# Kernel tuning notes

Measured on AMD Instinct MI355X. Metric: run time of the kernel, lower is better.

The kernel has to match this reference:

```python
import jax, jax.numpy as jnp
import numpy as np

MAX_LEN, BATCH, D_IN, D_H = 512, 128, 512, 512


def setup_inputs() -> dict:
    key = jax.random.key(0)
    ks = jax.random.split(key, 9)
    s_in = 1.0 / np.sqrt(D_IN)
    s_h = 1.0 / np.sqrt(D_H)
    return {
        "seq": jax.random.normal(ks[0], (MAX_LEN, BATCH, D_IN), jnp.float32),
        "W_iz": jax.random.normal(ks[1], (D_H, D_IN), jnp.float32) * s_in,
        "b_iz": jax.random.normal(ks[2], (D_H,), jnp.float32) * s_in,
        "W_in": jax.random.normal(ks[3], (D_H, D_IN), jnp.float32) * s_in,
        "b_in": jax.random.normal(ks[4], (D_H,), jnp.float32) * s_in,
        "W_hz": jax.random.normal(ks[5], (D_H, D_H), jnp.float32) * s_h,
        "b_hz": jax.random.normal(ks[6], (D_H,), jnp.float32) * s_h,
        "W_hn": jax.random.normal(ks[7], (D_H, D_H), jnp.float32) * s_h,
        "b_hn": jax.random.normal(ks[8], (D_H,), jnp.float32) * s_h,
    }


def reference(seq, W_iz, b_iz, W_in, b_in, W_hz, b_hz, W_hn, b_hn):
    # Precompute input projections for all timesteps in one big GEMM each.
    # iz, inn: [max_len, batch, hidden]
    iz = jnp.einsum("tbi,hi->tbh", seq, W_iz) + b_iz
    inn = jnp.einsum("tbi,hi->tbh", seq, W_in) + b_in
    h0 = jnp.zeros((seq.shape[1], W_hz.shape[0]), seq.dtype)

    def step(h_prev, xs):
        iz_t, in_t = xs
        z_t = jax.nn.sigmoid(iz_t + h_prev @ W_hz.T + b_hz)
        # NOTE: original module sets r_t = ones, so no reset gating.
        n_t = jnp.tanh(in_t + (h_prev @ W_hn.T + b_hn))
        h_t = (1.0 - z_t) * n_t + z_t * h_prev
        return h_t, h_t

    _, H = jax.lax.scan(step, h0, (iz, inn))  # H: [max_len, batch, hidden]
    return H[None]  # [1, max_len, batch, hidden] (H.unsqueeze(0))
```

## Files before the change

### kernel.cpp

```cpp
#include <hip/hip_runtime.h>
#include <stdint.h>

typedef _Float16 f16x8 __attribute__((ext_vector_type(8)));
typedef _Float16 f16x4 __attribute__((ext_vector_type(4)));
typedef float    f32x4 __attribute__((ext_vector_type(4)));
typedef unsigned int u32x4v __attribute__((ext_vector_type(4)));

#define T_LEN 512
#define RLX   __ATOMIC_RELAXED
#define AGT   __HIP_MEMORY_SCOPE_AGENT

union PK4 { _Float16 h[4]; unsigned long long q; };
union QZ  { unsigned long long q; f16x4 v; };

__device__ __forceinline__ void gload_lds16(const void* gsrc, void* ldsdst) {
    auto g = (const __attribute__((address_space(1))) void*)(reinterpret_cast<uintptr_t>(gsrc));
    auto s = (__attribute__((address_space(3))) void*)(reinterpret_cast<uintptr_t>(ldsdst));
    __builtin_amdgcn_global_load_lds(g, s, 16, 0, 0);
}

__global__ __launch_bounds__(256) void prep_misc(
    const float* __restrict__ W_iz, const float* __restrict__ W_in,
    const float* __restrict__ W_hz, const float* __restrict__ W_hn,
    const float* __restrict__ b_iz, const float* __restrict__ b_in,
    const float* __restrict__ b_hz, const float* __restrict__ b_hn,
    _Float16* __restrict__ Wci, _Float16* __restrict__ Whc,
    float* __restrict__ bc, unsigned int* __restrict__ hbuf32)
{
    const int tid = blockIdx.x * 256 + threadIdx.x;
    if (tid < 131072) {
        const bool is_h = tid >= 65536;
        const int u = tid & 65535;
        const int e = u * 8;
        const int row = e >> 9;
        const int k = e & 511;
        const float* s;
        if (!is_h) s = (row < 512) ? (W_iz + (size_t)row * 512 + k)
                                   : (W_in + (size_t)(row - 512) * 512 + k);
        else       s = (row < 512) ? (W_hz + (size_t)row * 512 + k)
                                   : (W_hn + (size_t)(row - 512) * 512 + k);
        f32x4 a = *(const f32x4*)s;
        f32x4 b = *(const f32x4*)(s + 4);
        f16x8 o;
        o[0] = (_Float16)a[0]; o[1] = (_Float16)a[1];
        o[2] = (_Float16)a[2]; o[3] = (_Float16)a[3];
        o[4] = (_Float16)b[0]; o[5] = (_Float16)b[1];
        o[6] = (_Float16)b[2]; o[7] = (_Float16)b[3];
        _Float16* d = is_h ? Whc : Wci;
        *(f16x8*)(d + e) = o;
    } else if (tid < 132096) {
        const int j2 = tid - 131072;
        bc[j2] = (j2 < 512) ? (b_iz[j2] + b_hz[j2]) : (b_in[j2 - 512] + b_hn[j2 - 512]);
    } else if (tid < 164864) {
        const int u = tid - 132096;
        u32x4v z = {0u, 0u, 0u, 0u};
        *(u32x4v*)(hbuf32 + (size_t)u * 4) = z;
    }
}

__global__ __launch_bounds__(256) void gemm_proj(
    const float* __restrict__ A,
    const _Float16* __restrict__ Bw,
    const float* __restrict__ bc,
    _Float16* Co)
{
    __shared__ _Float16 As[128 * 40];
    __shared__ _Float16 Bs[128 * 32];

    const int mt = blockIdx.x;
    const int nt = blockIdx.y;
    const int m0 = mt * 128, n0 = nt * 128;
    const int tid = threadIdx.x;
    const int w = tid >> 6, l = tid & 63;
    const int wr = w >> 1, wc = w & 1;
    const int lrow = l & 15, lk = l >> 4;

    f32x4 acc[4][4] = {};

    const int arow = tid >> 1;
    const int acol = (tid & 1) * 16;

    for (int kt = 0; kt < 16; ++kt) {
        const int k0 = kt * 32;
        if (kt) __syncthreads();
        const float* as = A + (size_t)(m0 + arow) * 512 + k0 + acol;
        f32x4 a0 = *(const f32x4*)as;
        f32x4 a1 = *(const f32x4*)(as + 4);
        f32x4 a2 = *(const f32x4*)(as + 8);
        f32x4 a3 = *(const f32x4*)(as + 12);
        f16x8 h0, h1;
#pragma unroll
        for (int e = 0; e < 4; ++e) {
            h0[e] = (_Float16)a0[e]; h0[4 + e] = (_Float16)a1[e];
            h1[e] = (_Float16)a2[e]; h1[4 + e] = (_Float16)a3[e];
        }
        *(f16x8*)&As[arow * 40 + acol] = h0;
        *(f16x8*)&As[arow * 40 + acol + 8] = h1;
#pragma unroll
        for (int i = 0; i < 2; ++i) {
            const int chunk = w * 2 + i;
            const _Float16* gsrc =
                Bw + (size_t)(n0 + chunk * 16 + (l >> 2)) * 512 + k0 + (l & 3) * 8;
            gload_lds16(gsrc, &Bs[chunk * 512]);
        }
        __syncthreads();
        f16x8 af[4], bf[4];
#pragma unroll
        for (int i = 0; i < 4; ++i) {
            af[i] = *(const f16x8*)&As[(wr * 64 + i * 16 + lrow) * 40 + lk * 8];
            bf[i] = *(const f16x8*)&Bs[(wc * 64 + i * 16 + lrow) * 32 + lk * 8];
        }
#pragma unroll
        for (int mi = 0; mi < 4; ++mi)
#pragma unroll
            for (int ni = 0; ni < 4; ++ni)
                acc[mi][ni] = __builtin_amdgcn_mfma_f32_16x16x32_f16(
                    bf[ni], af[mi], acc[mi][ni], 0, 0, 0);
    }
    const int gate = nt >> 2;
#pragma unroll
    for (int mi = 0; mi < 4; ++mi) {
#pragma unroll
        for (int p = 0; p < 2; ++p) {
            const int j2q0 = n0 + wc * 64 + p * 32 + 4 * lk;
            const f32x4 b0 = *(const f32x4*)&bc[j2q0];
            const f32x4 b1 = *(const f32x4*)&bc[j2q0 + 16];
            f16x8 o;
#pragma unroll
            for (int r = 0; r < 4; ++r) {
                o[r]     = (_Float16)(acc[mi][2 * p][r]     + b0[r]);
                o[4 + r] = (_Float16)(acc[mi][2 * p + 1][r] + b1[r]);
            }
            const int blk_s = (wr * 4 + mi) * 16 + (nt & 3) * 4 + wc * 2 + p;
            _Float16* dst = Co + ((((size_t)mt * 128 + blk_s) * 2 + gate) * 512) + l * 8;
            *(f16x8*)dst = o;
        }
    }
}

__global__ __launch_bounds__(512, 1) void gru_scan(
    const _Float16* __restrict__ Whc,
    const char* izb,
    float* Hout,
    unsigned int* hbuf32)
{
    __shared__ _Float16 hlds[2 * 16 * 512];

    const int blk  = blockIdx.x;
    const int g    = blk & 7;
    const int slot = blk >> 3;
    const int tid  = threadIdx.x;
    const int wv   = tid >> 6;
    const int l    = tid & 63;
    const int lrow = l & 15, lk = l >> 4;
    const int jbase = slot * 128 + wv * 16;
    const int jq    = jbase + 4 * lk;
    const int bg    = 16 * g + lrow;
    const int blk_s = 16 * g + 4 * slot + (wv >> 1);
    const int stage_b = tid >> 5;
    const int stage_jq = 4 * (tid & 31);

    f16x8 wz[16], wn[16];
#pragma unroll
    for (int s = 0; s < 16; ++s) {
        wz[s] = *(const f16x8*)&Whc[(size_t)(jbase + lrow) * 512 + s * 32 + lk * 8];
        wn[s] = *(const f16x8*)&Whc[(size_t)(512 + jbase + lrow) * 512 + s * 32 + lk * 8];
    }

    *(unsigned long long*)&hlds[(lrow * 512 + jq) ^ ((lrow & 7) << 3)] = 0ull;

    QZ ez, en, oz, on;
    {
        const char* r0 = izb + ((size_t)0 * 128 + blk_s) * 2048 + l * 16 + (wv & 1) * 8;
        ez.q = *(const unsigned long long*)r0;
        en.q = *(const unsigned long long*)(r0 + 1024);
        const char* r1 = izb + ((size_t)1 * 128 + blk_s) * 2048 + l * 16 + (wv & 1) * 8;
        oz.q = *(const unsigned long long*)r1;
        on.q = *(const unsigned long long*)(r1 + 1024);
    }

    float hm[4] = {0.f, 0.f, 0.f, 0.f};

    const unsigned long long* hb64base = (const unsigned long long*)hbuf32;

    auto step = [&](int t, QZ& cz, QZ& cn) {
        const int par = (t + 1) & 1;
        const int lp  = t & 1;
        const unsigned long long tp =
            (unsigned long long)(unsigned)t | ((unsigned long long)(unsigned)t << 32);

        const unsigned long long* hb64 = hb64base + (size_t)par * 32768;
        unsigned long long q0[3], q1[3];
        int pix[3];
#pragma unroll
        for (int i = 0; i < 3; ++i) {
            const int s_i = (slot + 1 + i) & 3;
            const int u32i = (16 * g + stage_b) * 512 + s_i * 128 + stage_jq;
            pix[i] = u32i >> 1;
            q0[i] = __hip_atomic_load(hb64 + pix[i],     RLX, AGT);
            q1[i] = __hip_atomic_load(hb64 + pix[i] + 1, RLX, AGT);
        }
        while (true) {
            unsigned long long x = 0;
#pragma unroll
            for (int i = 0; i < 3; ++i)
                x |= (q0[i] ^ tp) | (q1[i] ^ tp);
            if (__all((x & 0x0000FFFF0000FFFFull) == 0)) break;
#pragma unroll
            for (int i = 0; i < 3; ++i) {
                q0[i] = __hip_atomic_load(hb64 + pix[i],     RLX, AGT);
                q1[i] = __hip_atomic_load(hb64 + pix[i] + 1, RLX, AGT);
            }
        }

#pragma unroll
        for (int i = 0; i < 3; ++i) {
            const int s_i = (slot + 1 + i) & 3;
            const unsigned int w0 = ((unsigned int)(q0[i] >> 16)) & 0xFFFFu;
            const unsigned int w1 = (unsigned int)(q0[i] >> 48);
            const unsigned int w2 = ((unsigned int)(q1[i] >> 16)) & 0xFFFFu;
            const unsigned int w3 = (unsigned int)(q1[i] >> 48);
            const unsigned long long out =
                (unsigned long long)(w0 | (w1 << 16)) |
                ((unsigned long long)(w2 | (w3 << 16)) << 32);
            const int idx = (lp * 8192 + stage_b * 512 + s_i * 128 + stage_jq)
                            ^ ((stage_b & 7) << 3);
            *(unsigned long long*)&hlds[idx] = out;
        }

        __syncthreads();

        f32x4 az = {0.f, 0.f, 0.f, 0.f}, an = {0.f, 0.f, 0.f, 0.f};
        const int hbase = lp * 8192 + lrow * 512;
        const int sw = (lrow & 7) << 3;
#pragma unroll
        for (int s = 0; s < 16; ++s) {
            asm volatile("" : "+v"(wz[s]), "+v"(wn[s]));
            const f16x8 hf = *(const f16x8*)&hlds[(hbase + s * 32 + lk * 8) ^ sw];
            az = __builtin_amdgcn_mfma_f32_16x16x32_f16(wz[s], hf, az, 0, 0, 0);
            an = __builtin_amdgcn_mfma_f32_16x16x32_f16(wn[s], hf, an, 0, 0, 0);
        }

        PK4 own;
        f32x4 Hv;
#pragma unroll
        for (int r = 0; r < 4; ++r) {
            float zpre = az[r] + (float)cz.v[r];
            float npre = an[r] + (float)cn.v[r];
            zpre = fminf(fmaxf(zpre, -30.f), 30.f);
            const float z = 1.f / (1.f + __expf(-zpre));
            npre = fminf(fmaxf(npre, -15.f), 15.f);
            const float e2 = __expf(2.f * npre);
            const float n = (e2 - 1.f) / (e2 + 1.f);
            hm[r] = (1.f - z) * n + z * hm[r];
            Hv[r] = hm[r];
            own.h[r] = (_Float16)hm[r];
        }

        if (t + 2 < T_LEN) {
            const char* rec = izb + ((size_t)(t + 2) * 128 + blk_s) * 2048
                              + l * 16 + (wv & 1) * 8;
            cz.q = *(const unsigned long long*)rec;
            cn.q = *(const unsigned long long*)(rec + 1024);
        }
        __builtin_amdgcn_sched_barrier(0);

        *(unsigned long long*)
            &hlds[(((t + 1) & 1) * 8192 + lrow * 512 + jq) ^ ((lrow & 7) << 3)] = own.q;

        if (t < T_LEN - 1) {
            if (t + 2 < T_LEN) {
                asm volatile("s_waitcnt vmcnt(2)" ::: "memory");
            } else {
                asm volatile("s_waitcnt vmcnt(0)" ::: "memory");
            }
            __builtin_amdgcn_sched_barrier(0);
            const unsigned long long tagp =
                (unsigned long long)(unsigned)(t + 1) |
                ((unsigned long long)(unsigned)(t + 1) << 32);
            const unsigned long long d0 =
                ((own.q & 0xFFFFull) << 16) |
                (((own.q >> 16) & 0xFFFFull) << 48) | tagp;
            const unsigned long long d1 =
                (((own.q >> 32) & 0xFFFFull) << 16) |
                (((own.q >> 48) & 0xFFFFull) << 48) | tagp;
            unsigned long long* hw = (unsigned long long*)
                (hbuf32 + (size_t)(t & 1) * 65536 + (size_t)bg * 512 + jq);
            __hip_atomic_store(hw,     d0, RLX, AGT);
            __hip_atomic_store(hw + 1, d1, RLX, AGT);
        }

        *(f32x4*)&Hout[(size_t)t * 65536 + (size_t)bg * 512 + jq] = Hv;
    };

    for (int t = 0; t < T_LEN; t += 2) {
        step(t,     ez, en);
        step(t + 1, oz, on);
    }
}

extern "C" void kernel_launch(void* const* d_in, const int* in_sizes, int n_in,
                              void* d_out, int out_size, void* d_ws, size_t ws_size,
                              hipStream_t stream) {
    (void)in_sizes; (void)n_in; (void)out_size; (void)ws_size;
    const float* seq  = (const float*)d_in[0];
    const float* W_iz = (const float*)d_in[1];
    const float* b_iz = (const float*)d_in[2];
    const float* W_in = (const float*)d_in[3];
    const float* b_in = (const float*)d_in[4];
    const float* W_hz = (const float*)d_in[5];
    const float* b_hz = (const float*)d_in[6];
    const float* W_hn = (const float*)d_in[7];
    const float* b_hn = (const float*)d_in[8];

    char* ws = (char*)d_ws;
    _Float16*     Wci    = (_Float16*)(ws);
    _Float16*     Whc    = (_Float16*)(ws + 1048576);
    float*        bc     = (float*)   (ws + 2097152);
    unsigned int* hbuf32 = (unsigned int*)(ws + 2101248);

    prep_misc<<<644, 256, 0, stream>>>(W_iz, W_in, W_hz, W_hn,
                                       b_iz, b_in, b_hz, b_hn,
                                       Wci, Whc, bc, hbuf32);
    gemm_proj<<<dim3(512, 8), 256, 0, stream>>>(seq, Wci, bc, (_Float16*)d_out);
    gru_scan<<<32, 512, 0, stream>>>(Whc, (const char*)d_out, (float*)d_out, hbuf32);
}
```

Before: 1.827 ms.

## Spread GRU scan over 128 small blocks with recurrent weights staged in LDS

The recurrent scan moves from 32 blocks of 512 threads to 128 blocks of 128 threads. Each block now owns 32 hidden units for a 16-row batch group, and its W_hz/W_hn slice is loaded into LDS with global_load_lds instead of being held in registers. The aim is to use more compute units and cut per-block MFMA work per timestep. In exchange, each block must poll 15 peer slices instead of 3 in the cross-block h exchange, which raises spin-wait traffic and synchronisation latency on every step, and weights are reread from LDS on each step.

```diff
diff --git a/kernel.cpp b/kernel.cpp
--- a/kernel.cpp
+++ b/kernel.cpp
@@ -138,12 +138,13 @@
     }
 }
 
-__global__ __launch_bounds__(512, 1) void gru_scan(
+__global__ __launch_bounds__(128, 1) void gru_scan(
     const _Float16* __restrict__ Whc,
     const char* izb,
     float* Hout,
     unsigned int* hbuf32)
 {
+    __shared__ _Float16 wlds[64 * 512];
     __shared__ _Float16 hlds[2 * 16 * 512];
 
     const int blk  = blockIdx.x;
@@ -153,34 +154,36 @@
     const int wv   = tid >> 6;
     const int l    = tid & 63;
     const int lrow = l & 15, lk = l >> 4;
-    const int jbase = slot * 128 + wv * 16;
-    const int jq    = jbase + 4 * lk;
-    const int bg    = 16 * g + lrow;
-    const int blk_s = 16 * g + 4 * slot + (wv >> 1);
-    const int stage_b = tid >> 5;
-    const int stage_jq = 4 * (tid & 31);
-
-    f16x8 wz[16], wn[16];
-#pragma unroll
-    for (int s = 0; s < 16; ++s) {
-        wz[s] = *(const f16x8*)&Whc[(size_t)(jbase + lrow) * 512 + s * 32 + lk * 8];
-        wn[s] = *(const f16x8*)&Whc[(size_t)(512 + jbase + lrow) * 512 + s * 32 + lk * 8];
-    }
+    const int j0   = slot * 32;
+    const int jq   = j0 + wv * 16 + 4 * lk;
+    const int bg   = 16 * g + lrow;
+    const int blk_s = 16 * g + slot;
+    const int stage_b = tid >> 3;
+    const int stage_j = (tid & 7) * 4;
+
+    for (int gate = 0; gate < 2; ++gate)
+#pragma unroll
+        for (int s = 0; s < 16; ++s) {
+            const _Float16* gsrc = Whc +
+                (size_t)(gate * 512 + j0 + wv * 16 + lrow) * 512 + s * 32 + lk * 8;
+            gload_lds16(gsrc, &wlds[((wv * 2 + gate) * 16 + s) * 512]);
+        }
 
     *(unsigned long long*)&hlds[(lrow * 512 + jq) ^ ((lrow & 7) << 3)] = 0ull;
 
     QZ ez, en, oz, on;
     {
-        const char* r0 = izb + ((size_t)0 * 128 + blk_s) * 2048 + l * 16 + (wv & 1) * 8;
-        ez.q = *(const unsigned long long*)r0;
-        en.q = *(const unsigned long long*)(r0 + 1024);
-        const char* r1 = izb + ((size_t)1 * 128 + blk_s) * 2048 + l * 16 + (wv & 1) * 8;
-        oz.q = *(const unsigned long long*)r1;
-        on.q = *(const unsigned long long*)(r1 + 1024);
-    }
+        const char* rec = izb + (size_t)blk_s * 2048 + l * 16 + wv * 8;
+        ez.q = *(const unsigned long long*)(rec);
+        en.q = *(const unsigned long long*)(rec + 1024);
+        oz.q = *(const unsigned long long*)(rec + 262144);
+        on.q = *(const unsigned long long*)(rec + 262144 + 1024);
+    }
+
+    asm volatile("s_waitcnt vmcnt(0)" ::: "memory");
+    __syncthreads();
 
     float hm[4] = {0.f, 0.f, 0.f, 0.f};
-
     const unsigned long long* hb64base = (const unsigned long long*)hbuf32;
 
     auto step = [&](int t, QZ& cz, QZ& cn) {
@@ -190,12 +193,12 @@
             (unsigned long long)(unsigned)t | ((unsigned long long)(unsigned)t << 32);
 
         const unsigned long long* hb64 = hb64base + (size_t)par * 32768;
-        unsigned long long q0[3], q1[3];
-        int pix[3];
-#pragma unroll
-        for (int i = 0; i < 3; ++i) {
-            const int s_i = (slot + 1 + i) & 3;
-            const int u32i = (16 * g + stage_b) * 512 + s_i * 128 + stage_jq;
+        unsigned long long q0[15], q1[15];
+        int pix[15];
+#pragma unroll
+        for (int i = 0; i < 15; ++i) {
+            const int s_i = (slot + 1 + i) & 15;
+            const int u32i = (16 * g + stage_b) * 512 + s_i * 32 + stage_j;
             pix[i] = u32i >> 1;
             q0[i] = __hip_atomic_load(hb64 + pix[i],     RLX, AGT);
             q1[i] = __hip_atomic_load(hb64 + pix[i] + 1, RLX, AGT);
@@ -203,19 +206,19 @@
         while (true) {
             unsigned long long x = 0;
 #pragma unroll
-            for (int i = 0; i < 3; ++i)
+            for (int i = 0; i < 15; ++i)
                 x |= (q0[i] ^ tp) | (q1[i] ^ tp);
             if (__all((x & 0x0000FFFF0000FFFFull) == 0)) break;
 #pragma unroll
-            for (int i = 0; i < 3; ++i) {
+            for (int i = 0; i < 15; ++i) {
                 q0[i] = __hip_atomic_load(hb64 + pix[i],     RLX, AGT);
                 q1[i] = __hip_atomic_load(hb64 + pix[i] + 1, RLX, AGT);
             }
         }
 
 #pragma unroll
-        for (int i = 0; i < 3; ++i) {
-            const int s_i = (slot + 1 + i) & 3;
+        for (int i = 0; i < 15; ++i) {
+            const int s_i = (slot + 1 + i) & 15;
             const unsigned int w0 = ((unsigned int)(q0[i] >> 16)) & 0xFFFFu;
             const unsigned int w1 = (unsigned int)(q0[i] >> 48);
             const unsigned int w2 = ((unsigned int)(q1[i] >> 16)) & 0xFFFFu;
@@ -223,7 +226,7 @@
             const unsigned long long out =
                 (unsigned long long)(w0 | (w1 << 16)) |
                 ((unsigned long long)(w2 | (w3 << 16)) << 32);
-            const int idx = (lp * 8192 + stage_b * 512 + s_i * 128 + stage_jq)
+            const int idx = (lp * 8192 + stage_b * 512 + s_i * 32 + stage_j)
                             ^ ((stage_b & 7) << 3);
             *(unsigned long long*)&hlds[idx] = out;
         }
@@ -235,10 +238,11 @@
         const int sw = (lrow & 7) << 3;
 #pragma unroll
         for (int s = 0; s < 16; ++s) {
-            asm volatile("" : "+v"(wz[s]), "+v"(wn[s]));
-            const f16x8 hf = *(const f16x8*)&hlds[(hbase + s * 32 + lk * 8) ^ sw];
-            az = __builtin_amdgcn_mfma_f32_16x16x32_f16(wz[s], hf, az, 0, 0, 0);
-            an = __builtin_amdgcn_mfma_f32_16x16x32_f16(wn[s], hf, an, 0, 0, 0);
+            const f16x8 wzv = *(const f16x8*)&wlds[((wv * 2 + 0) * 16 + s) * 512 + l * 8];
+            const f16x8 wnv = *(const f16x8*)&wlds[((wv * 2 + 1) * 16 + s) * 512 + l * 8];
+            const f16x8 hf  = *(const f16x8*)&hlds[(hbase + s * 32 + lk * 8) ^ sw];
+            az = __builtin_amdgcn_mfma_f32_16x16x32_f16(wzv, hf, az, 0, 0, 0);
+            an = __builtin_amdgcn_mfma_f32_16x16x32_f16(wnv, hf, an, 0, 0, 0);
         }
 
         PK4 own;
@@ -259,7 +263,7 @@
 
         if (t + 2 < T_LEN) {
             const char* rec = izb + ((size_t)(t + 2) * 128 + blk_s) * 2048
-                              + l * 16 + (wv & 1) * 8;
+                              + l * 16 + wv * 8;
             cz.q = *(const unsigned long long*)rec;
             cn.q = *(const unsigned long long*)(rec + 1024);
         }
@@ -323,5 +327,5 @@
                                        b_iz, b_in, b_hz, b_hn,
                                        Wci, Whc, bc, hbuf32);
     gemm_proj<<<dim3(512, 8), 256, 0, stream>>>(seq, Wci, bc, (_Float16*)d_out);
-    gru_scan<<<32, 512, 0, stream>>>(Whc, (const char*)d_out, (float*)d_out, hbuf32);
-}
+    gru_scan<<<128, 128, 0, stream>>>(Whc, (const char*)d_out, (float*)d_out, hbuf32);
+}
```

Result: slower. 2.483 ms (+36.0%).

## Split GRU scan across 64 blocks of 256 threads with weights staged in LDS

Applied to the files above, without the earlier changes.

The recurrent scan now runs on 64 workgroups of 4 waves instead of 32 of 8, so each block owns 64 hidden columns and exchanges h with 7 peer slots instead of 3. Recurrent weights move from registers into 128 KB of LDS, loaded asynchronously via global_load_lds, and the h buffer drops double-buffering in favour of an extra barrier before each refill. This spreads the per-step matmul over more CUs to shorten the serial critical path. In exchange there are more cross-block flag polls per step, extra LDS weight reads on every step, and an added barrier.

```diff
diff --git a/kernel.cpp b/kernel.cpp
--- a/kernel.cpp
+++ b/kernel.cpp
@@ -138,13 +138,14 @@
     }
 }
 
-__global__ __launch_bounds__(512, 1) void gru_scan(
+__global__ __launch_bounds__(256, 1) void gru_scan(
     const _Float16* __restrict__ Whc,
     const char* izb,
     float* Hout,
     unsigned int* hbuf32)
 {
-    __shared__ _Float16 hlds[2 * 16 * 512];
+    __shared__ _Float16 wlds[65536];
+    __shared__ _Float16 hlds[8192];
 
     const int blk  = blockIdx.x;
     const int g    = blk & 7;
@@ -153,49 +154,52 @@
     const int wv   = tid >> 6;
     const int l    = tid & 63;
     const int lrow = l & 15, lk = l >> 4;
-    const int jbase = slot * 128 + wv * 16;
+    const int jbase = slot * 64 + wv * 16;
     const int jq    = jbase + 4 * lk;
     const int bg    = 16 * g + lrow;
-    const int blk_s = 16 * g + 4 * slot + (wv >> 1);
-    const int stage_b = tid >> 5;
-    const int stage_jq = 4 * (tid & 31);
-
-    f16x8 wz[16], wn[16];
-#pragma unroll
-    for (int s = 0; s < 16; ++s) {
-        wz[s] = *(const f16x8*)&Whc[(size_t)(jbase + lrow) * 512 + s * 32 + lk * 8];
-        wn[s] = *(const f16x8*)&Whc[(size_t)(512 + jbase + lrow) * 512 + s * 32 + lk * 8];
-    }
-
-    *(unsigned long long*)&hlds[(lrow * 512 + jq) ^ ((lrow & 7) << 3)] = 0ull;
+    const int blk_s = 16 * g + 2 * slot + (wv >> 1);
+    const int stage_b = tid >> 4;
+    const int stage_jq = 4 * (tid & 15);
+    const int swl = (lrow & 7) << 3;
+    const int swb = (stage_b & 7) << 3;
+
+    for (int gate = 0; gate < 2; ++gate)
+#pragma unroll
+        for (int s = 0; s < 16; ++s) {
+            const _Float16* gsrc = Whc +
+                (size_t)(gate * 512 + jbase + lrow) * 512 + s * 32 + lk * 8;
+            gload_lds16(gsrc, &wlds[((wv * 2 + gate) * 16 + s) * 512]);
+        }
 
     QZ ez, en, oz, on;
     {
-        const char* r0 = izb + ((size_t)0 * 128 + blk_s) * 2048 + l * 16 + (wv & 1) * 8;
+        const char* r0 = izb + (size_t)blk_s * 2048 + l * 16 + (wv & 1) * 8;
         ez.q = *(const unsigned long long*)r0;
         en.q = *(const unsigned long long*)(r0 + 1024);
-        const char* r1 = izb + ((size_t)1 * 128 + blk_s) * 2048 + l * 16 + (wv & 1) * 8;
+        const char* r1 = r0 + 262144;
         oz.q = *(const unsigned long long*)r1;
         on.q = *(const unsigned long long*)(r1 + 1024);
     }
 
+    asm volatile("s_waitcnt vmcnt(0)" ::: "memory");
+    __syncthreads();
+
     float hm[4] = {0.f, 0.f, 0.f, 0.f};
-
+    unsigned long long own_q = 0ull;
     const unsigned long long* hb64base = (const unsigned long long*)hbuf32;
 
     auto step = [&](int t, QZ& cz, QZ& cn) {
         const int par = (t + 1) & 1;
-        const int lp  = t & 1;
         const unsigned long long tp =
             (unsigned long long)(unsigned)t | ((unsigned long long)(unsigned)t << 32);
 
         const unsigned long long* hb64 = hb64base + (size_t)par * 32768;
-        unsigned long long q0[3], q1[3];
-        int pix[3];
-#pragma unroll
-        for (int i = 0; i < 3; ++i) {
-            const int s_i = (slot + 1 + i) & 3;
-            const int u32i = (16 * g + stage_b) * 512 + s_i * 128 + stage_jq;
+        unsigned long long q0[7], q1[7];
+        int pix[7];
+#pragma unroll
+        for (int i = 0; i < 7; ++i) {
+            const int s_i = (slot + 1 + i) & 7;
+            const int u32i = (16 * g + stage_b) * 512 + s_i * 64 + stage_jq;
             pix[i] = u32i >> 1;
             q0[i] = __hip_atomic_load(hb64 + pix[i],     RLX, AGT);
             q1[i] = __hip_atomic_load(hb64 + pix[i] + 1, RLX, AGT);
@@ -203,19 +207,21 @@
         while (true) {
             unsigned long long x = 0;
 #pragma unroll
-            for (int i = 0; i < 3; ++i)
+            for (int i = 0; i < 7; ++i)
                 x |= (q0[i] ^ tp) | (q1[i] ^ tp);
             if (__all((x & 0x0000FFFF0000FFFFull) == 0)) break;
 #pragma unroll
-            for (int i = 0; i < 3; ++i) {
+            for (int i = 0; i < 7; ++i) {
                 q0[i] = __hip_atomic_load(hb64 + pix[i],     RLX, AGT);
                 q1[i] = __hip_atomic_load(hb64 + pix[i] + 1, RLX, AGT);
             }
         }
 
-#pragma unroll
-        for (int i = 0; i < 3; ++i) {
-            const int s_i = (slot + 1 + i) & 3;
+        __syncthreads();
+
+#pragma unroll
+        for (int i = 0; i < 7; ++i) {
+            const int s_i = (slot + 1 + i) & 7;
             const unsigned int w0 = ((unsigned int)(q0[i] >> 16)) & 0xFFFFu;
             const unsigned int w1 = (unsigned int)(q0[i] >> 48);
             const unsigned int w2 = ((unsigned int)(q1[i] >> 16)) & 0xFFFFu;
@@ -223,22 +229,21 @@
             const unsigned long long out =
                 (unsigned long long)(w0 | (w1 << 16)) |
                 ((unsigned long long)(w2 | (w3 << 16)) << 32);
-            const int idx = (lp * 8192 + stage_b * 512 + s_i * 128 + stage_jq)
-                            ^ ((stage_b & 7) << 3);
+            const int idx = (stage_b * 512 + s_i * 64 + stage_jq) ^ swb;
             *(unsigned long long*)&hlds[idx] = out;
         }
+        *(unsigned long long*)&hlds[(lrow * 512 + jq) ^ swl] = own_q;
 
         __syncthreads();
 
         f32x4 az = {0.f, 0.f, 0.f, 0.f}, an = {0.f, 0.f, 0.f, 0.f};
-        const int hbase = lp * 8192 + lrow * 512;
-        const int sw = (lrow & 7) << 3;
 #pragma unroll
         for (int s = 0; s < 16; ++s) {
-            asm volatile("" : "+v"(wz[s]), "+v"(wn[s]));
-            const f16x8 hf = *(const f16x8*)&hlds[(hbase + s * 32 + lk * 8) ^ sw];
-            az = __builtin_amdgcn_mfma_f32_16x16x32_f16(wz[s], hf, az, 0, 0, 0);
-            an = __builtin_amdgcn_mfma_f32_16x16x32_f16(wn[s], hf, an, 0, 0, 0);
+            const f16x8 wzv = *(const f16x8*)&wlds[((wv * 2 + 0) * 16 + s) * 512 + l * 8];
+            const f16x8 wnv = *(const f16x8*)&wlds[((wv * 2 + 1) * 16 + s) * 512 + l * 8];
+            const f16x8 hf  = *(const f16x8*)&hlds[(lrow * 512 + s * 32 + lk * 8) ^ swl];
+            az = __builtin_amdgcn_mfma_f32_16x16x32_f16(wzv, hf, az, 0, 0, 0);
+            an = __builtin_amdgcn_mfma_f32_16x16x32_f16(wnv, hf, an, 0, 0, 0);
         }
 
         PK4 own;
@@ -256,6 +261,7 @@
             Hv[r] = hm[r];
             own.h[r] = (_Float16)hm[r];
         }
+        own_q = own.q;
 
         if (t + 2 < T_LEN) {
             const char* rec = izb + ((size_t)(t + 2) * 128 + blk_s) * 2048
@@ -265,25 +271,18 @@
         }
         __builtin_amdgcn_sched_barrier(0);
 
-        *(unsigned long long*)
-            &hlds[(((t + 1) & 1) * 8192 + lrow * 512 + jq) ^ ((lrow & 7) << 3)] = own.q;
-
         if (t < T_LEN - 1) {
-            if (t + 2 < T_LEN) {
-                asm volatile("s_waitcnt vmcnt(2)" ::: "memory");
-            } else {
-                asm volatile("s_waitcnt vmcnt(0)" ::: "memory");
-            }
+            asm volatile("s_waitcnt vmcnt(2)" ::: "memory");
             __builtin_amdgcn_sched_barrier(0);
             const unsigned long long tagp =
                 (unsigned long long)(unsigned)(t + 1) |
                 ((unsigned long long)(unsigned)(t + 1) << 32);
             const unsigned long long d0 =
-                ((own.q & 0xFFFFull) << 16) |
-                (((own.q >> 16) & 0xFFFFull) << 48) | tagp;
+                ((own_q & 0xFFFFull) << 16) |
+                (((own_q >> 16) & 0xFFFFull) << 48) | tagp;
             const unsigned long long d1 =
-                (((own.q >> 32) & 0xFFFFull) << 16) |
-                (((own.q >> 48) & 0xFFFFull) << 48) | tagp;
+                (((own_q >> 32) & 0xFFFFull) << 16) |
+                (((own_q >> 48) & 0xFFFFull) << 48) | tagp;
             unsigned long long* hw = (unsigned long long*)
                 (hbuf32 + (size_t)(t & 1) * 65536 + (size_t)bg * 512 + jq);
             __hip_atomic_store(hw,     d0, RLX, AGT);
@@ -323,5 +322,5 @@
                                        b_iz, b_in, b_hz, b_hn,
                                        Wci, Whc, bc, hbuf32);
     gemm_proj<<<dim3(512, 8), 256, 0, stream>>>(seq, Wci, bc, (_Float16*)d_out);
-    gru_scan<<<32, 512, 0, stream>>>(Whc, (const char*)d_out, (float*)d_out, hbuf32);
-}
+    gru_scan<<<64, 256, 0, stream>>>(Whc, (const char*)d_out, (float*)d_out, hbuf32);
+}
```

Result: slower. 2.014 ms (+10.2%).
